# Kernel optimization log

Hardware: AMD Instinct MI355X
Metric: run time of the kernel (lower is better)

## Reference

```python
import jax, jax.numpy as jnp
import numpy as np

D = 128        # feature_dims
ITERS = 2      # update_iters
B, R = 8, 256  # n segments (proteins), residues per segment
NEG_SLOPE = 0.1

def leaky(x):
    return jax.nn.leaky_relu(x, NEG_SLOPE)

def setup_inputs() -> dict:
    key = jax.random.key(0)
    ks = jax.random.split(key, 13)
    def w(k, shape):
        fan_in = shape[0]
        return jax.random.normal(k, shape, jnp.float32) / np.sqrt(fan_in)
    return {
        "fresidues": jax.random.normal(ks[0], (B, R, 20), jnp.float32),
        "coordinates": jax.random.normal(ks[1], (B, R, 3), jnp.float32) * 10.0,
        "W_emb": w(ks[2], (20, D)),                    # res_embedding (no bias)
        "W_e1": w(ks[3], (2 * D + 1, D)),              # linear_e layer 1
        "b_e1": jnp.zeros((D,), jnp.float32),
        "W_e2": w(ks[4], (D, D)),                      # linear_e layer 2
        "b_e2": jnp.zeros((D,), jnp.float32),
        "W_inf": w(ks[5], (D, 1)),                     # linear_inf gate
        "b_inf": jnp.zeros((1,), jnp.float32),
        "W_h1": w(ks[6], (2 * D, D)),                  # linear_h layer 1
        "b_h1": jnp.zeros((D,), jnp.float32),
        "W_h2": w(ks[7], (D, D)),                      # linear_h layer 2
        "b_h2": jnp.zeros((D,), jnp.float32),
    }

def reference(fresidues, coordinates, W_emb, W_e1, b_e1, W_e2, b_e2,
              W_inf, b_inf, W_h1, b_h1, W_h2, b_h2):
    # h: [B,R,D]
    h = leaky(fresidues @ W_emb)
    # pairwise squared distances: [B,R,R,1], constant across iterations
    d2 = jnp.sum(jnp.square(coordinates[:, :, None, :] - coordinates[:, None, :, :]),
                 axis=-1, keepdims=True)
    # mask out self-edges (1 - eye): [1,R,R,1]
    mask = (1.0 - jnp.eye(R, dtype=h.dtype))[None, :, :, None]
    # split edge-MLP first-layer weights to avoid materializing the [B,R,R,2D+1] concat:
    # m_input = cat([h_i, h_j, d2]) @ W_e1  ==  h_i@W_i + h_j@W_j + d2*w_d
    W_i, W_j, w_d = W_e1[:D], W_e1[D:2 * D], W_e1[2 * D]
    for _ in range(ITERS):
        ti = h @ W_i                                   # [B,R,D] receiver part
        tj = h @ W_j                                   # [B,R,D] sender part
        pre = ti[:, :, None, :] + tj[:, None, :, :] + d2 * w_d + b_e1  # [B,R,R,D]
        m = leaky(leaky(pre) @ W_e2 + b_e2)            # [B,R,R,D]
        e = jax.nn.sigmoid(m @ W_inf + b_inf) * mask   # [B,R,R,1]
        m_pre = jnp.sum(m * e, axis=2)                 # sum over senders j -> [B,R,D]
        hm = jnp.concatenate([h, m_pre], axis=-1)      # [B,R,2D]
        h = (leaky(hm @ W_h1 + b_h1) @ W_h2 + b_h2) + h
    return h

if __name__ == "__main__":
    out = reference(**setup_inputs())
    print(out.shape, out.dtype)
```

## Files before the change

### kernel.cpp

```cpp
#include <hip/hip_runtime.h>

typedef unsigned short ushort_t;
typedef __attribute__((ext_vector_type(8))) short shortx8;
typedef __attribute__((ext_vector_type(4))) float floatx4;
typedef __attribute__((ext_vector_type(2))) float floatx2;

#define NS 0.1f

__device__ __forceinline__ ushort_t f2bf_rne(float f) {
  union { float f; unsigned int u; } v; v.f = f;
  unsigned int r = v.u + 0x7FFFu + ((v.u >> 16) & 1u);
  return (ushort_t)(r >> 16);
}
__device__ __forceinline__ unsigned int pk2bf(float a, float b) {
  union { float f; unsigned int u; } x, y; x.f = a; y.f = b;
  return __builtin_amdgcn_perm(y.u + 0x8000u, x.u + 0x8000u, 0x07060302u);
}
__device__ __forceinline__ ushort_t f2bf_rhu(float f) {
  union { float f; unsigned int u; } v; v.f = f;
  return (ushort_t)((v.u + 0x8000u) >> 16);
}
__device__ __forceinline__ float lk(float x) { return fmaxf(x, NS * x); }
__device__ __forceinline__ floatx2 lk2(floatx2 v) {
  return __builtin_elementwise_max(v, v * (floatx2){NS, NS});
}

__global__ __launch_bounds__(256) void prep_w(
    const float* __restrict__ W_e1, const float* __restrict__ W_e2,
    const float* __restrict__ W_h1, const float* __restrict__ W_h2,
    ushort_t* __restrict__ wijf, ushort_t* __restrict__ we2f,
    ushort_t* __restrict__ wh1f, ushort_t* __restrict__ wh2f) {
  int e = blockIdx.x * 256 + threadIdx.x;
  int which, le;
  if (e < 32768) { which = 0; le = e; }
  else if (e < 49152) { which = 1; le = e - 32768; }
  else if (e < 81920) { which = 2; le = e - 49152; }
  else { which = 3; le = e - 81920; }
  const int NT = (which == 0) ? 16 : 8;
  int f = le >> 3, j = le & 7;
  int lane = f & 63, ft = f >> 6;
  int t = ft % NT, s = ft / NT;
  int n = t * 16 + (lane & 15), k = s * 32 + (lane >> 4) * 8 + j;
  float v; ushort_t* d;
  if (which == 0) { v = (n < 128) ? W_e1[k * 128 + n] : W_e1[(128 + k) * 128 + (n - 128)]; d = wijf; }
  else if (which == 1) { v = W_e2[k * 128 + n]; d = we2f; }
  else if (which == 2) { v = W_h1[k * 128 + n]; d = wh1f; }
  else { v = W_h2[k * 128 + n]; d = wh2f; }
  d[le] = f2bf_rne(v);
}

__device__ __forceinline__ void proj_store(float v, int m, int n,
                                           float* __restrict__ ti, float* __restrict__ tjf) {
  if (n < 128) {
    ti[(size_t)m * 128 + n] = v;
  } else {
    int k = n - 128, b = m >> 8, j = m & 255;
    int s = k >> 5, lg2 = (k >> 3) & 3, j8 = k & 7;
    tjf[((((size_t)(b * 4 + s)) * 256 + j) * 4 + lg2) * 8 + j8] = v;
  }
}

__global__ __launch_bounds__(256) void h0_proj(
    const float* __restrict__ fres, const float* __restrict__ Wemb,
    const ushort_t* __restrict__ wijf, float* __restrict__ h_out,
    float* __restrict__ ti, float* __restrict__ tjf) {
  const int m0 = blockIdx.x * 16;
  const int tid = threadIdx.x;
  const int w = tid >> 6, lane = tid & 63, l16 = lane & 15, lg = lane >> 4;
  __shared__ __align__(16) ushort_t sH[16][136];
  {
    const int row = tid >> 4, c0 = (tid & 15) * 8;
    const float* fr = fres + (size_t)(m0 + row) * 20;
    float a[8] = {0, 0, 0, 0, 0, 0, 0, 0};
    for (int k = 0; k < 20; ++k) {
      float fv = fr[k];
      float4 w0 = *(const float4*)(Wemb + k * 128 + c0);
      float4 w1 = *(const float4*)(Wemb + k * 128 + c0 + 4);
      a[0] += fv * w0.x; a[1] += fv * w0.y; a[2] += fv * w0.z; a[3] += fv * w0.w;
      a[4] += fv * w1.x; a[5] += fv * w1.y; a[6] += fv * w1.z; a[7] += fv * w1.w;
    }
#pragma unroll
    for (int x = 0; x < 8; ++x) a[x] = lk(a[x]);
    float* ho = h_out + (size_t)(m0 + row) * 128 + c0;
    *(float4*)ho = (float4){a[0], a[1], a[2], a[3]};
    *(float4*)(ho + 4) = (float4){a[4], a[5], a[6], a[7]};
    unsigned int* sh = (unsigned int*)&sH[row][c0];
    sh[0] = pk2bf(a[0], a[1]); sh[1] = pk2bf(a[2], a[3]);
    sh[2] = pk2bf(a[4], a[5]); sh[3] = pk2bf(a[6], a[7]);
  }
  __syncthreads();
  floatx4 ap[4];
#pragma unroll
  for (int q = 0; q < 4; ++q) ap[q] = (floatx4){0.f, 0.f, 0.f, 0.f};
  const shortx8* Wp = (const shortx8*)wijf;
#pragma unroll
  for (int s = 0; s < 4; ++s) {
    shortx8 af = *(const shortx8*)&sH[l16][s * 32 + lg * 8];
#pragma unroll
    for (int q = 0; q < 4; ++q)
      ap[q] = __builtin_amdgcn_mfma_f32_16x16x32_bf16(af, Wp[(s * 16 + 4 * w + q) * 64 + lane], ap[q], 0, 0, 0);
  }
#pragma unroll
  for (int q = 0; q < 4; ++q) {
    const int n = (4 * w + q) * 16 + l16;
#pragma unroll
    for (int r = 0; r < 4; ++r) proj_store(ap[q][r], m0 + lg * 4 + r, n, ti, tjf);
  }
}

__global__ __launch_bounds__(256, 3) void edge_kernel(
    const float* __restrict__ ti, const float* __restrict__ tjf,
    const float* __restrict__ coords, const ushort_t* __restrict__ we2f,
    const float* __restrict__ W_e1, const float* __restrict__ b_e1,
    const float* __restrict__ b_e2, const float* __restrict__ W_inf,
    const float* __restrict__ b_inf, float* __restrict__ mp0, float* __restrict__ mp1) {
  const int blk = blockIdx.x;
  const int b = blk >> 9, i = (blk >> 1) & 255, ch = blk & 1;
  const int tid = threadIdx.x;
  const int w = tid >> 6, lane = tid & 63, l16 = lane & 15, lg = lane >> 4;

  __shared__ __align__(16) ushort_t sW[16384];
  __shared__ __align__(16) float sTiP[128];
  __shared__ __align__(16) float sWd[128];
  __shared__ __align__(16) float sD2[128];
  __shared__ __align__(16) float sMp[4][128];

  {
    shortx8* dst = (shortx8*)sW;
    const shortx8* src = (const shortx8*)we2f;
#pragma unroll
    for (int r = 0; r < 8; ++r) dst[r * 256 + tid] = src[r * 256 + tid];
  }
  if (tid < 128) {
    sTiP[tid] = ti[(size_t)(b * 256 + i) * 128 + tid] + b_e1[tid];
    sWd[tid] = W_e1[256 * 128 + tid];
    const int j = ch * 128 + tid;
    float dx = coords[(size_t)(b * 256 + i) * 3 + 0] - coords[(size_t)(b * 256 + j) * 3 + 0];
    float dy = coords[(size_t)(b * 256 + i) * 3 + 1] - coords[(size_t)(b * 256 + j) * 3 + 1];
    float dz = coords[(size_t)(b * 256 + i) * 3 + 2] - coords[(size_t)(b * 256 + j) * 3 + 2];
    sD2[tid] = dx * dx + dy * dy + dz * dz;
  }
  floatx4 acc[2][8];
#pragma unroll
  for (int t = 0; t < 8; ++t) {
    float bv = b_e2[t * 16 + l16];
    acc[0][t] = (floatx4){bv, bv, bv, bv};
    acc[1][t] = acc[0][t];
  }
  __syncthreads();

  float d2a[2];
  d2a[0] = sD2[w * 16 + l16];
  d2a[1] = sD2[64 + w * 16 + l16];
  const shortx8* sWf = (const shortx8*)sW;

#pragma unroll
  for (int s = 0; s < 4; ++s) {
    const int k0 = s * 32 + lg * 8;
    floatx2 p2[4], w2[4];
#pragma unroll
    for (int x = 0; x < 4; ++x) {
      p2[x] = *(const floatx2*)&sTiP[k0 + 2 * x];
      w2[x] = *(const floatx2*)&sWd[k0 + 2 * x];
    }
    shortx8 af[2];
#pragma unroll
    for (int c = 0; c < 2; ++c) {
      const int jr = ch * 128 + c * 64 + w * 16 + l16;
      const float* tb = tjf + (((size_t)(b * 4 + s) * 256 + jr) * 4 + lg) * 8;
      float4 t0 = *(const float4*)tb;
      float4 t1 = *(const float4*)(tb + 4);
      const floatx2 d2v = (floatx2){d2a[c], d2a[c]};
      floatx2 pr0 = (floatx2){t0.x, t0.y} + (p2[0] + d2v * w2[0]);
      floatx2 pr1 = (floatx2){t0.z, t0.w} + (p2[1] + d2v * w2[1]);
      floatx2 pr2 = (floatx2){t1.x, t1.y} + (p2[2] + d2v * w2[2]);
      floatx2 pr3 = (floatx2){t1.z, t1.w} + (p2[3] + d2v * w2[3]);
      floatx2 l0 = lk2(pr0), l1 = lk2(pr1), l2 = lk2(pr2), l3 = lk2(pr3);
      union { shortx8 s8; unsigned int u[4]; } A;
      A.u[0] = pk2bf(l0.x, l0.y); A.u[1] = pk2bf(l1.x, l1.y);
      A.u[2] = pk2bf(l2.x, l2.y); A.u[3] = pk2bf(l3.x, l3.y);
      af[c] = A.s8;
    }
#pragma unroll
    for (int tg = 0; tg < 2; ++tg) {
      shortx8 b0 = sWf[(s * 8 + tg * 4 + 0) * 64 + lane];
      shortx8 b1 = sWf[(s * 8 + tg * 4 + 1) * 64 + lane];
      shortx8 b2 = sWf[(s * 8 + tg * 4 + 2) * 64 + lane];
      shortx8 b3 = sWf[(s * 8 + tg * 4 + 3) * 64 + lane];
#pragma unroll
      for (int c = 0; c < 2; ++c) {
        acc[c][tg * 4 + 0] = __builtin_amdgcn_mfma_f32_16x16x32_bf16(af[c], b0, acc[c][tg * 4 + 0], 0, 0, 0);
        acc[c][tg * 4 + 1] = __builtin_amdgcn_mfma_f32_16x16x32_bf16(af[c], b1, acc[c][tg * 4 + 1], 0, 0, 0);
        acc[c][tg * 4 + 2] = __builtin_amdgcn_mfma_f32_16x16x32_bf16(af[c], b2, acc[c][tg * 4 + 2], 0, 0, 0);
        acc[c][tg * 4 + 3] = __builtin_amdgcn_mfma_f32_16x16x32_bf16(af[c], b3, acc[c][tg * 4 + 3], 0, 0, 0);
      }
    }
  }

  float winfv[8], mp[8];
#pragma unroll
  for (int t = 0; t < 8; ++t) { winfv[t] = W_inf[t * 16 + l16]; mp[t] = 0.f; }
  const float binf = b_inf[0];
#pragma unroll
  for (int c = 0; c < 2; ++c) {
#pragma unroll
    for (int t = 0; t < 8; ++t) {
      floatx2 v0 = lk2((floatx2){acc[c][t][0], acc[c][t][1]});
      floatx2 v1 = lk2((floatx2){acc[c][t][2], acc[c][t][3]});
      acc[c][t][0] = v0.x; acc[c][t][1] = v0.y; acc[c][t][2] = v1.x; acc[c][t][3] = v1.y;
    }
    float p[4];
#pragma unroll
    for (int r = 0; r < 4; ++r) {
      float sum = 0.f;
#pragma unroll
      for (int t = 0; t < 8; ++t) sum += acc[c][t][r] * winfv[t];
      p[r] = sum;
    }
#pragma unroll
    for (int off = 1; off <= 8; off <<= 1)
#pragma unroll
      for (int r = 0; r < 4; ++r) p[r] += __shfl_xor(p[r], off);
#pragma unroll
    for (int r = 0; r < 4; ++r) {
      const int jg = ch * 128 + c * 64 + w * 16 + lg * 4 + r;
      float x = p[r] + binf;
      float e = __builtin_amdgcn_rcpf(1.f + __expf(-x));
      if (jg == i) e = 0.f;
#pragma unroll
      for (int t = 0; t < 8; ++t) mp[t] += acc[c][t][r] * e;
    }
  }
#pragma unroll
  for (int t = 0; t < 8; ++t) {
    mp[t] += __shfl_xor(mp[t], 16);
    mp[t] += __shfl_xor(mp[t], 32);
  }
  if (lg == 0) {
#pragma unroll
    for (int t = 0; t < 8; ++t) sMp[w][t * 16 + l16] = mp[t];
  }
  __syncthreads();
  if (tid < 128) {
    float v = sMp[0][tid] + sMp[1][tid] + sMp[2][tid] + sMp[3][tid];
    float* mpo = ch ? mp1 : mp0;
    mpo[(size_t)(b * 256 + i) * 128 + tid] = v;
  }
}

__global__ __launch_bounds__(256) void node_kernel(
    const float* __restrict__ h_in, const float* __restrict__ mp0, const float* __restrict__ mp1,
    const ushort_t* __restrict__ wh1f, const float* __restrict__ b_h1,
    const ushort_t* __restrict__ wh2f, const float* __restrict__ b_h2,
    const ushort_t* __restrict__ wijf, float* __restrict__ h_out,
    float* __restrict__ ti, float* __restrict__ tjf, const int do_proj) {
  const int m0 = blockIdx.x * 16;
  const int tid = threadIdx.x;
  const int w = tid >> 6, lane = tid & 63, l16 = lane & 15, lg = lane >> 4;
  __shared__ __align__(16) ushort_t sA[16][264];
  __shared__ __align__(16) ushort_t sU[16][136];
  __shared__ __align__(16) ushort_t sHp[16][136];

  {
    const int row = tid >> 4, c0 = (tid & 15) * 16;
    unsigned int* dst = (unsigned int*)&sA[row][c0];
    if (c0 < 128) {
      const float* src = h_in + (size_t)(m0 + row) * 128 + c0;
#pragma unroll
      for (int x = 0; x < 8; ++x) dst[x] = pk2bf(src[2 * x], src[2 * x + 1]);
    } else {
      const float* s0 = mp0 + (size_t)(m0 + row) * 128 + (c0 - 128);
      const float* s1 = mp1 + (size_t)(m0 + row) * 128 + (c0 - 128);
#pragma unroll
      for (int x = 0; x < 8; ++x)
        dst[x] = pk2bf(s0[2 * x] + s1[2 * x], s0[2 * x + 1] + s1[2 * x + 1]);
    }
  }
  __syncthreads();
  floatx4 au[2];
#pragma unroll
  for (int q = 0; q < 2; ++q) { float bv = b_h1[(2 * w + q) * 16 + l16]; au[q] = (floatx4){bv, bv, bv, bv}; }
  const shortx8* W1 = (const shortx8*)wh1f;
#pragma unroll
  for (int s = 0; s < 8; ++s) {
    shortx8 af = *(const shortx8*)&sA[l16][s * 32 + lg * 8];
#pragma unroll
    for (int q = 0; q < 2; ++q)
      au[q] = __builtin_amdgcn_mfma_f32_16x16x32_bf16(af, W1[(s * 8 + 2 * w + q) * 64 + lane], au[q], 0, 0, 0);
  }
#pragma unroll
  for (int q = 0; q < 2; ++q)
#pragma unroll
    for (int r = 0; r < 4; ++r)
      sU[lg * 4 + r][(2 * w + q) * 16 + l16] = f2bf_rhu(lk(au[q][r]));
  __syncthreads();
  floatx4 ah[2];
#pragma unroll
  for (int q = 0; q < 2; ++q) { float bv = b_h2[(2 * w + q) * 16 + l16]; ah[q] = (floatx4){bv, bv, bv, bv}; }
  const shortx8* W2 = (const shortx8*)wh2f;
#pragma unroll
  for (int s = 0; s < 4; ++s) {
    shortx8 af = *(const shortx8*)&sU[l16][s * 32 + lg * 8];
#pragma unroll
    for (int q = 0; q < 2; ++q)
      ah[q] = __builtin_amdgcn_mfma_f32_16x16x32_bf16(af, W2[(s * 8 + 2 * w + q) * 64 + lane], ah[q], 0, 0, 0);
  }
#pragma unroll
  for (int q = 0; q < 2; ++q) {
    const int n = (2 * w + q) * 16 + l16;
#pragma unroll
    for (int r = 0; r < 4; ++r) {
      const int m = m0 + lg * 4 + r;
      float v = ah[q][r] + h_in[(size_t)m * 128 + n];
      h_out[(size_t)m * 128 + n] = v;
      sHp[lg * 4 + r][n] = f2bf_rhu(v);
    }
  }
  if (!do_proj) return;
  __syncthreads();
  floatx4 ap[4];
#pragma unroll
  for (int q = 0; q < 4; ++q) ap[q] = (floatx4){0.f, 0.f, 0.f, 0.f};
  const shortx8* Wp = (const shortx8*)wijf;
#pragma unroll
  for (int s = 0; s < 4; ++s) {
    shortx8 af = *(const shortx8*)&sHp[l16][s * 32 + lg * 8];
#pragma unroll
    for (int q = 0; q < 4; ++q)
      ap[q] = __builtin_amdgcn_mfma_f32_16x16x32_bf16(af, Wp[(s * 16 + 4 * w + q) * 64 + lane], ap[q], 0, 0, 0);
  }
#pragma unroll
  for (int q = 0; q < 4; ++q) {
    const int n = (4 * w + q) * 16 + l16;
#pragma unroll
    for (int r = 0; r < 4; ++r) proj_store(ap[q][r], m0 + lg * 4 + r, n, ti, tjf);
  }
}

extern "C" void kernel_launch(void* const* d_in, const int* in_sizes, int n_in,
                              void* d_out, int out_size, void* d_ws, size_t ws_size,
                              hipStream_t stream) {
  const float* fres   = (const float*)d_in[0];
  const float* coords = (const float*)d_in[1];
  const float* W_emb  = (const float*)d_in[2];
  const float* W_e1   = (const float*)d_in[3];
  const float* b_e1   = (const float*)d_in[4];
  const float* W_e2   = (const float*)d_in[5];
  const float* b_e2   = (const float*)d_in[6];
  const float* W_inf  = (const float*)d_in[7];
  const float* b_inf  = (const float*)d_in[8];
  const float* W_h1   = (const float*)d_in[9];
  const float* b_h1   = (const float*)d_in[10];
  const float* W_h2   = (const float*)d_in[11];
  const float* b_h2   = (const float*)d_in[12];
  float* out = (float*)d_out;

  char* ws = (char*)d_ws;
  float* hA  = (float*)(ws + (0 << 20));
  float* hB  = (float*)(ws + (1 << 20));
  float* tib = (float*)(ws + (2 << 20));
  float* tjf = (float*)(ws + (3 << 20));
  float* mp0 = (float*)(ws + (4 << 20));
  float* mp1 = (float*)(ws + (5 << 20));
  ushort_t* wijf = (ushort_t*)(ws + (6 << 20));
  ushort_t* we2f = wijf + 32768;
  ushort_t* wh1f = we2f + 16384;
  ushort_t* wh2f = wh1f + 32768;

  prep_w<<<384, 256, 0, stream>>>(W_e1, W_e2, W_h1, W_h2, wijf, we2f, wh1f, wh2f);
  h0_proj<<<128, 256, 0, stream>>>(fres, W_emb, wijf, hA, tib, tjf);

  edge_kernel<<<4096, 256, 0, stream>>>(tib, tjf, coords, we2f, W_e1, b_e1, b_e2, W_inf, b_inf, mp0, mp1);
  node_kernel<<<128, 256, 0, stream>>>(hA, mp0, mp1, wh1f, b_h1, wh2f, b_h2, wijf, hB, tib, tjf, 1);

  edge_kernel<<<4096, 256, 0, stream>>>(tib, tjf, coords, we2f, W_e1, b_e1, b_e2, W_inf, b_inf, mp0, mp1);
  node_kernel<<<128, 256, 0, stream>>>(hB, mp0, mp1, wh1f, b_h1, wh2f, b_h2, wijf, out, tib, tjf, 0);
}
```

Baseline: 180.2 us.

## Process two receiver rows per edge block with tjf prefetch

```diff
diff --git a/kernel.cpp b/kernel.cpp
--- a/kernel.cpp
+++ b/kernel.cpp
@@ -115,15 +115,15 @@
     const float* __restrict__ b_e2, const float* __restrict__ W_inf,
     const float* __restrict__ b_inf, float* __restrict__ mp0, float* __restrict__ mp1) {
   const int blk = blockIdx.x;
-  const int b = blk >> 9, i = (blk >> 1) & 255, ch = blk & 1;
+  const int b = blk >> 8, ip = (blk >> 1) & 127, ch = blk & 1;
   const int tid = threadIdx.x;
   const int w = tid >> 6, lane = tid & 63, l16 = lane & 15, lg = lane >> 4;
 
   __shared__ __align__(16) ushort_t sW[16384];
-  __shared__ __align__(16) float sTiP[128];
+  __shared__ __align__(16) float sTiP[2][128];
   __shared__ __align__(16) float sWd[128];
-  __shared__ __align__(16) float sD2[128];
-  __shared__ __align__(16) float sMp[4][128];
+  __shared__ __align__(16) float sD2[2][128];
+  __shared__ __align__(16) float sMp[2][4][128];
 
   {
     shortx8* dst = (shortx8*)sW;
@@ -131,120 +131,159 @@
 #pragma unroll
     for (int r = 0; r < 8; ++r) dst[r * 256 + tid] = src[r * 256 + tid];
   }
-  if (tid < 128) {
-    sTiP[tid] = ti[(size_t)(b * 256 + i) * 128 + tid] + b_e1[tid];
-    sWd[tid] = W_e1[256 * 128 + tid];
-    const int j = ch * 128 + tid;
+  {
+    const int ii = tid >> 7, t2 = tid & 127;
+    const int i = ip * 2 + ii;
+    sTiP[ii][t2] = ti[(size_t)(b * 256 + i) * 128 + t2] + b_e1[t2];
+    if (ii == 0) sWd[t2] = W_e1[256 * 128 + t2];
+    const int j = ch * 128 + t2;
     float dx = coords[(size_t)(b * 256 + i) * 3 + 0] - coords[(size_t)(b * 256 + j) * 3 + 0];
     float dy = coords[(size_t)(b * 256 + i) * 3 + 1] - coords[(size_t)(b * 256 + j) * 3 + 1];
     float dz = coords[(size_t)(b * 256 + i) * 3 + 2] - coords[(size_t)(b * 256 + j) * 3 + 2];
-    sD2[tid] = dx * dx + dy * dy + dz * dz;
-  }
-  floatx4 acc[2][8];
+    sD2[ii][t2] = dx * dx + dy * dy + dz * dz;
+  }
+  float bev[8], winfv[8];
 #pragma unroll
   for (int t = 0; t < 8; ++t) {
-    float bv = b_e2[t * 16 + l16];
-    acc[0][t] = (floatx4){bv, bv, bv, bv};
-    acc[1][t] = acc[0][t];
-  }
-  __syncthreads();
-
-  float d2a[2];
-  d2a[0] = sD2[w * 16 + l16];
-  d2a[1] = sD2[64 + w * 16 + l16];
+    bev[t] = b_e2[t * 16 + l16];
+    winfv[t] = W_inf[t * 16 + l16];
+  }
+  const float binf = b_inf[0];
+  __syncthreads();
+
   const shortx8* sWf = (const shortx8*)sW;
 
 #pragma unroll
-  for (int s = 0; s < 4; ++s) {
-    const int k0 = s * 32 + lg * 8;
-    floatx2 p2[4], w2[4];
-#pragma unroll
-    for (int x = 0; x < 4; ++x) {
-      p2[x] = *(const floatx2*)&sTiP[k0 + 2 * x];
-      w2[x] = *(const floatx2*)&sWd[k0 + 2 * x];
-    }
-    shortx8 af[2];
+  for (int ii = 0; ii < 2; ++ii) {
+    const int i = ip * 2 + ii;
+    float d2a[2];
+    d2a[0] = sD2[ii][w * 16 + l16];
+    d2a[1] = sD2[ii][64 + w * 16 + l16];
+
+    floatx4 acc[2][8];
+#pragma unroll
+    for (int t = 0; t < 8; ++t) {
+      acc[0][t] = (floatx4){bev[t], bev[t], bev[t], bev[t]};
+      acc[1][t] = acc[0][t];
+    }
+
+    float4 cur0[2], cur1[2];
 #pragma unroll
     for (int c = 0; c < 2; ++c) {
       const int jr = ch * 128 + c * 64 + w * 16 + l16;
-      const float* tb = tjf + (((size_t)(b * 4 + s) * 256 + jr) * 4 + lg) * 8;
-      float4 t0 = *(const float4*)tb;
-      float4 t1 = *(const float4*)(tb + 4);
-      const floatx2 d2v = (floatx2){d2a[c], d2a[c]};
-      floatx2 pr0 = (floatx2){t0.x, t0.y} + (p2[0] + d2v * w2[0]);
-      floatx2 pr1 = (floatx2){t0.z, t0.w} + (p2[1] + d2v * w2[1]);
-      floatx2 pr2 = (floatx2){t1.x, t1.y} + (p2[2] + d2v * w2[2]);
-      floatx2 pr3 = (floatx2){t1.z, t1.w} + (p2[3] + d2v * w2[3]);
-      floatx2 l0 = lk2(pr0), l1 = lk2(pr1), l2 = lk2(pr2), l3 = lk2(pr3);
-      union { shortx8 s8; unsigned int u[4]; } A;
-      A.u[0] = pk2bf(l0.x, l0.y); A.u[1] = pk2bf(l1.x, l1.y);
-      A.u[2] = pk2bf(l2.x, l2.y); A.u[3] = pk2bf(l3.x, l3.y);
-      af[c] = A.s8;
-    }
-#pragma unroll
-    for (int tg = 0; tg < 2; ++tg) {
-      shortx8 b0 = sWf[(s * 8 + tg * 4 + 0) * 64 + lane];
-      shortx8 b1 = sWf[(s * 8 + tg * 4 + 1) * 64 + lane];
-      shortx8 b2 = sWf[(s * 8 + tg * 4 + 2) * 64 + lane];
-      shortx8 b3 = sWf[(s * 8 + tg * 4 + 3) * 64 + lane];
+      const float* tb = tjf + (((size_t)(b * 4 + 0) * 256 + jr) * 4 + lg) * 8;
+      cur0[c] = *(const float4*)tb;
+      cur1[c] = *(const float4*)(tb + 4);
+    }
+
+#pragma unroll
+    for (int s = 0; s < 4; ++s) {
+      float4 nxt0[2], nxt1[2];
+      if (s < 3) {
+#pragma unroll
+        for (int c = 0; c < 2; ++c) {
+          const int jr = ch * 128 + c * 64 + w * 16 + l16;
+          const float* tb = tjf + (((size_t)(b * 4 + s + 1) * 256 + jr) * 4 + lg) * 8;
+          nxt0[c] = *(const float4*)tb;
+          nxt1[c] = *(const float4*)(tb + 4);
+        }
+      }
+      const int k0 = s * 32 + lg * 8;
+      floatx2 p2[4], w2[4];
+#pragma unroll
+      for (int x = 0; x < 4; ++x) {
+        p2[x] = *(const floatx2*)&sTiP[ii][k0 + 2 * x];
+        w2[x] = *(const floatx2*)&sWd[k0 + 2 * x];
+      }
+      shortx8 af[2];
 #pragma unroll
       for (int c = 0; c < 2; ++c) {
-        acc[c][tg * 4 + 0] = __builtin_amdgcn_mfma_f32_16x16x32_bf16(af[c], b0, acc[c][tg * 4 + 0], 0, 0, 0);
-        acc[c][tg * 4 + 1] = __builtin_amdgcn_mfma_f32_16x16x32_bf16(af[c], b1, acc[c][tg * 4 + 1], 0, 0, 0);
-        acc[c][tg * 4 + 2] = __builtin_amdgcn_mfma_f32_16x16x32_bf16(af[c], b2, acc[c][tg * 4 + 2], 0, 0, 0);
-        acc[c][tg * 4 + 3] = __builtin_amdgcn_mfma_f32_16x16x32_bf16(af[c], b3, acc[c][tg * 4 + 3], 0, 0, 0);
-      }
-    }
-  }
-
-  float winfv[8], mp[8];
-#pragma unroll
-  for (int t = 0; t < 8; ++t) { winfv[t] = W_inf[t * 16 + l16]; mp[t] = 0.f; }
-  const float binf = b_inf[0];
-#pragma unroll
-  for (int c = 0; c < 2; ++c) {
+        const floatx2 d2v = (floatx2){d2a[c], d2a[c]};
+        floatx2 pr0 = (floatx2){cur0[c].x, cur0[c].y} + (p2[0] + d2v * w2[0]);
+        floatx2 pr1 = (floatx2){cur0[c].z, cur0[c].w} + (p2[1] + d2v * w2[1]);
+        floatx2 pr2 = (floatx2){cur1[c].x, cur1[c].y} + (p2[2] + d2v * w2[2]);
+        floatx2 pr3 = (floatx2){cur1[c].z, cur1[c].w} + (p2[3] + d2v * w2[3]);
+        floatx2 l0 = lk2(pr0), l1 = lk2(pr1), l2 = lk2(pr2), l3 = lk2(pr3);
+        union { shortx8 s8; unsigned int u[4]; } A;
+        A.u[0] = pk2bf(l0.x, l0.y); A.u[1] = pk2bf(l1.x, l1.y);
+        A.u[2] = pk2bf(l2.x, l2.y); A.u[3] = pk2bf(l3.x, l3.y);
+        af[c] = A.s8;
+      }
+#pragma unroll
+      for (int tg = 0; tg < 2; ++tg) {
+        shortx8 b0 = sWf[(s * 8 + tg * 4 + 0) * 64 + lane];
+        shortx8 b1 = sWf[(s * 8 + tg * 4 + 1) * 64 + lane];
+        shortx8 b2 = sWf[(s * 8 + tg * 4 + 2) * 64 + lane];
+        shortx8 b3 = sWf[(s * 8 + tg * 4 + 3) * 64 + lane];
+#pragma unroll
+        for (int c = 0; c < 2; ++c) {
+          acc[c][tg * 4 + 0] = __builtin_amdgcn_mfma_f32_16x16x32_bf16(af[c], b0, acc[c][tg * 4 + 0], 0, 0, 0);
+          acc[c][tg * 4 + 1] = __builtin_amdgcn_mfma_f32_16x16x32_bf16(af[c], b1, acc[c][tg * 4 + 1], 0, 0, 0);
+          acc[c][tg * 4 + 2] = __builtin_amdgcn_mfma_f32_16x16x32_bf16(af[c], b2, acc[c][tg * 4 + 2], 0, 0, 0);
+          acc[c][tg * 4 + 3] = __builtin_amdgcn_mfma_f32_16x16x32_bf16(af[c], b3, acc[c][tg * 4 + 3], 0, 0, 0);
+        }
+      }
+#pragma unroll
+      for (int c = 0; c < 2; ++c) { cur0[c] = nxt0[c]; cur1[c] = nxt1[c]; }
+    }
+
+    floatx2 mpp[8];
+#pragma unroll
+    for (int t = 0; t < 8; ++t) mpp[t] = (floatx2){0.f, 0.f};
+#pragma unroll
+    for (int c = 0; c < 2; ++c) {
+#pragma unroll
+      for (int t = 0; t < 8; ++t) {
+        floatx2 v0 = lk2((floatx2){acc[c][t][0], acc[c][t][1]});
+        floatx2 v1 = lk2((floatx2){acc[c][t][2], acc[c][t][3]});
+        acc[c][t][0] = v0.x; acc[c][t][1] = v0.y; acc[c][t][2] = v1.x; acc[c][t][3] = v1.y;
+      }
+      floatx2 q01 = (floatx2){0.f, 0.f}, q23 = (floatx2){0.f, 0.f};
+#pragma unroll
+      for (int t = 0; t < 8; ++t) {
+        const floatx2 wv = (floatx2){winfv[t], winfv[t]};
+        q01 += (floatx2){acc[c][t][0], acc[c][t][1]} * wv;
+        q23 += (floatx2){acc[c][t][2], acc[c][t][3]} * wv;
+      }
+      float p[4] = {q01.x, q01.y, q23.x, q23.y};
+#pragma unroll
+      for (int off = 1; off <= 8; off <<= 1)
+#pragma unroll
+        for (int r = 0; r < 4; ++r) p[r] += __shfl_xor(p[r], off);
+      float e[4];
+#pragma unroll
+      for (int r = 0; r < 4; ++r) {
+        const int jg = ch * 128 + c * 64 + w * 16 + lg * 4 + r;
+        float x = p[r] + binf;
+        e[r] = __builtin_amdgcn_rcpf(1.f + __expf(-x));
+        if (jg == i) e[r] = 0.f;
+      }
+      const floatx2 e01 = (floatx2){e[0], e[1]}, e23 = (floatx2){e[2], e[3]};
+#pragma unroll
+      for (int t = 0; t < 8; ++t) {
+        mpp[t] += (floatx2){acc[c][t][0], acc[c][t][1]} * e01;
+        mpp[t] += (floatx2){acc[c][t][2], acc[c][t][3]} * e23;
+      }
+    }
+    float mp[8];
 #pragma unroll
     for (int t = 0; t < 8; ++t) {
-      floatx2 v0 = lk2((floatx2){acc[c][t][0], acc[c][t][1]});
-      floatx2 v1 = lk2((floatx2){acc[c][t][2], acc[c][t][3]});
-      acc[c][t][0] = v0.x; acc[c][t][1] = v0.y; acc[c][t][2] = v1.x; acc[c][t][3] = v1.y;
-    }
-    float p[4];
-#pragma unroll
-    for (int r = 0; r < 4; ++r) {
-      float sum = 0.f;
-#pragma unroll
-      for (int t = 0; t < 8; ++t) sum += acc[c][t][r] * winfv[t];
-      p[r] = sum;
-    }
-#pragma unroll
-    for (int off = 1; off <= 8; off <<= 1)
-#pragma unroll
-      for (int r = 0; r < 4; ++r) p[r] += __shfl_xor(p[r], off);
-#pragma unroll
-    for (int r = 0; r < 4; ++r) {
-      const int jg = ch * 128 + c * 64 + w * 16 + lg * 4 + r;
-      float x = p[r] + binf;
-      float e = __builtin_amdgcn_rcpf(1.f + __expf(-x));
-      if (jg == i) e = 0.f;
-#pragma unroll
-      for (int t = 0; t < 8; ++t) mp[t] += acc[c][t][r] * e;
-    }
-  }
-#pragma unroll
-  for (int t = 0; t < 8; ++t) {
-    mp[t] += __shfl_xor(mp[t], 16);
-    mp[t] += __shfl_xor(mp[t], 32);
-  }
-  if (lg == 0) {
-#pragma unroll
-    for (int t = 0; t < 8; ++t) sMp[w][t * 16 + l16] = mp[t];
-  }
-  __syncthreads();
-  if (tid < 128) {
-    float v = sMp[0][tid] + sMp[1][tid] + sMp[2][tid] + sMp[3][tid];
+      mp[t] = mpp[t].x + mpp[t].y;
+      mp[t] += __shfl_xor(mp[t], 16);
+      mp[t] += __shfl_xor(mp[t], 32);
+    }
+    if (lg == 0) {
+#pragma unroll
+      for (int t = 0; t < 8; ++t) sMp[ii][w][t * 16 + l16] = mp[t];
+    }
+  }
+  __syncthreads();
+  {
+    const int ii = tid >> 7, t2 = tid & 127;
+    const int i = ip * 2 + ii;
+    float v = sMp[ii][0][t2] + sMp[ii][1][t2] + sMp[ii][2][t2] + sMp[ii][3][t2];
     float* mpo = ch ? mp1 : mp0;
-    mpo[(size_t)(b * 256 + i) * 128 + tid] = v;
+    mpo[(size_t)(b * 256 + i) * 128 + t2] = v;
   }
 }
 
@@ -370,9 +409,9 @@
   prep_w<<<384, 256, 0, stream>>>(W_e1, W_e2, W_h1, W_h2, wijf, we2f, wh1f, wh2f);
   h0_proj<<<128, 256, 0, stream>>>(fres, W_emb, wijf, hA, tib, tjf);
 
-  edge_kernel<<<4096, 256, 0, stream>>>(tib, tjf, coords, we2f, W_e1, b_e1, b_e2, W_inf, b_inf, mp0, mp1);
+  edge_kernel<<<2048, 256, 0, stream>>>(tib, tjf, coords, we2f, W_e1, b_e1, b_e2, W_inf, b_inf, mp0, mp1);
   node_kernel<<<128, 256, 0, stream>>>(hA, mp0, mp1, wh1f, b_h1, wh2f, b_h2, wijf, hB, tib, tjf, 1);
 
-  edge_kernel<<<4096, 256, 0, stream>>>(tib, tjf, coords, we2f, W_e1, b_e1, b_e2, W_inf, b_inf, mp0, mp1);
+  edge_kernel<<<2048, 256, 0, stream>>>(tib, tjf, coords, we2f, W_e1, b_e1, b_e2, W_inf, b_inf, mp0, mp1);
   node_kernel<<<128, 256, 0, stream>>>(hB, mp0, mp1, wh1f, b_h1, wh2f, b_h2, wijf, out, tib, tjf, 0);
 }
```

New measurement: 180.7 us. Within noise of the previous version (+0.3%).
